# Performance work log

Measured on AMD Instinct MI355X. Metric: run time of the kernel, lower is better.

The kernel has to match this reference:

```python
import jax, jax.numpy as jnp
import numpy as np

B, D, H = 4096, 66, 512  # batch, system dim (22 atoms * 3), MLP hidden


def _dynamics(t, xs, W1, b1, W2, b2, W3, b3):
    # CNF vector field f(t, x): 3-layer SiLU MLP on concat([x, t])
    h = jnp.concatenate([xs, t], axis=1)          # [B, D+1]
    h = jax.nn.silu(h @ W1 + b1)                  # [B, H]
    h = jax.nn.silu(h @ W2 + b2)                  # [B, H]
    return h @ W3 + b3                            # [B, D]


def setup_inputs() -> dict:
    key = jax.random.key(0)
    ks = jax.random.split(key, 5)
    xs = jax.random.normal(ks[0], (B, D), dtype=jnp.float32)
    t = jax.random.uniform(ks[1], (B, 1), dtype=jnp.float32)
    W1 = jax.random.normal(ks[2], (D + 1, H), dtype=jnp.float32) / np.float32(np.sqrt(D + 1))
    b1 = jnp.zeros((H,), dtype=jnp.float32)
    W2 = jax.random.normal(ks[3], (H, H), dtype=jnp.float32) / np.float32(np.sqrt(H))
    b2 = jnp.zeros((H,), dtype=jnp.float32)
    W3 = jax.random.normal(ks[4], (H, D), dtype=jnp.float32) / np.float32(np.sqrt(H))
    b3 = jnp.zeros((D,), dtype=jnp.float32)
    return {"xs": xs, "t": t, "W1": W1, "b1": b1, "W2": W2, "b2": b2, "W3": W3, "b3": b3}


def reference(xs, t, W1, b1, W2, b2, W3, b3):
    # Exact divergence: trace of Jacobian d f / d x, computed with D JVPs
    # (forward-mode equivalent of the torch per-dim autograd.grad loop).
    def f(x):
        return _dynamics(t, x, W1, b1, W2, b2, W3, b3)

    dxs = f(xs)                                   # [B, D]
    eye = jnp.eye(D, dtype=xs.dtype)              # basis vectors e_i

    def jvp_col(e):
        _, tang = jax.jvp(f, (xs,), (jnp.broadcast_to(e, xs.shape),))
        return tang                               # J @ e_i, shape [B, D]

    tangs = jax.vmap(jvp_col)(eye)                # [D, B, D]
    div = jnp.einsum('dbd->b', tangs)             # sum_i (J e_i)_i = tr(J)
    return dxs, -div[:, None]
```

## Files before the change

kernel.cpp:

```cpp
#include <hip/hip_runtime.h>

#define Bn 4096
#define Dn 66
#define Hn 512

typedef __attribute__((ext_vector_type(8))) short short8;
typedef __attribute__((ext_vector_type(4))) float f32x4;

__device__ __forceinline__ unsigned short f2bf(float x) {
    union { float f; unsigned u; } v; v.f = x;
    unsigned r = v.u + 0x7fffu + ((v.u >> 16) & 1u);
    return (unsigned short)(r >> 16);
}
__device__ __forceinline__ float bf2f(unsigned short h) {
    union { float f; unsigned u; } v; v.u = ((unsigned)h) << 16; return v.f;
}


__global__ __launch_bounds__(512, 2) void k_pack(
    const float* __restrict__ W1, const float* __restrict__ W2,
    const float* __restrict__ W3,
    unsigned short* __restrict__ WQ, unsigned short* __restrict__ W3P)
{
    __shared__ float sLds[16*68];
    const int bid = blockIdx.x, tid = threadIdx.x;
    const int lane = tid & 63, wv = tid >> 6;

    if (bid < 64) {
        const int pb = bid;
        const int ct = pb >> 1;
        {
            const int r = tid >> 5, ii = tid & 31;
            const float* src = &W3[(size_t)(ct*16 + r)*Dn];
            sLds[r*68 + ii] = src[ii];
            sLds[r*68 + ii + 32] = src[ii + 32];
            if (ii < 2) sLds[r*68 + ii + 64] = src[ii + 64];
        }
        __syncthreads();
        const int ks = (pb & 1)*8 + wv;
        const int n = lane & 15, kg = lane >> 4;
        const int c = ct*16 + n;
        const int abase = ks*32 + kg*8;
        float w2v[8], m[8];
        #pragma unroll
        for (int j = 0; j < 8; ++j) {
            w2v[j] = W2[(size_t)(abase + j)*Hn + c];
            m[j] = 0.f;
        }
        #pragma unroll 2
        for (int i = 0; i < Dn; ++i) {
            const float w3 = sLds[n*68 + i];
            const float4 w1a = *(const float4*)&W1[(size_t)i*Hn + abase];
            const float4 w1b = *(const float4*)&W1[(size_t)i*Hn + abase + 4];
            m[0] = fmaf(w3, w1a.x, m[0]); m[1] = fmaf(w3, w1a.y, m[1]);
            m[2] = fmaf(w3, w1a.z, m[2]); m[3] = fmaf(w3, w1a.w, m[3]);
            m[4] = fmaf(w3, w1b.x, m[4]); m[5] = fmaf(w3, w1b.y, m[5]);
            m[6] = fmaf(w3, w1b.z, m[6]); m[7] = fmaf(w3, w1b.w, m[7]);
        }
        short8 pw, pc;
        #pragma unroll
        for (int j = 0; j < 8; ++j) {
            pw[j] = (short)f2bf(w2v[j]);
            pc[j] = (short)f2bf(w2v[j] * m[j]);
        }
        const size_t off = ((size_t)(ct*16 + ks)*64 + lane)*16;
        *(short8*)&WQ[off]     = pw;
        *(short8*)&WQ[off + 8] = pc;
    } else {
        const int tix = (bid - 64)*8 + wv;
        if (tix < 80) {
            const int ks = tix & 15;
            const int n = lane & 15;
            const int j_out = (tix >> 4)*16 + n;
            const int abase = ks*32 + (lane >> 4)*8;
            short8 p;
            #pragma unroll
            for (int j = 0; j < 8; ++j)
                p[j] = (j_out < Dn) ? (short)f2bf(W3[(size_t)(abase + j)*Dn + j_out]) : (short)0;
            *(short8*)&W3P[((size_t)tix*64 + lane)*8] = p;
        }
    }
}

__global__ __launch_bounds__(1024, 4) void k_fused(
    const float* __restrict__ xs, const float* __restrict__ tt,
    const float* __restrict__ W1, const float* __restrict__ b1,
    const unsigned short* __restrict__ WQ, const float* __restrict__ b2,
    const unsigned short* __restrict__ W3P, const float* __restrict__ b3,
    float* __restrict__ out)
{
    __shared__ float sX[67*16];
    __shared__ __align__(16) unsigned short sA[8192];
    __shared__ __align__(16) unsigned short sS[8192];
    __shared__ __align__(16) unsigned short sH[8192];
    __shared__ __align__(16) unsigned short sL[8192];
    __shared__ float sRed[16*16];

    const int tid = threadIdx.x, lane = tid & 63, wv = tid >> 6;
    const int rt = blockIdx.x, r0 = rt*16;
    const int n = lane & 15, kg = lane >> 4;
    const int rot = (rt >> 3) & 15;

    for (int idx = tid; idx < 67*16; idx += 1024) {
        const int i = idx >> 4, r = idx & 15;
        sX[idx] = (i < Dn) ? xs[(size_t)(r0+r)*Dn + i] : tt[r0+r];
    }
    __syncthreads();

    {
        const int rg = lane & 7, cg = lane >> 3;
        const int ks = wv;
        const int c0 = ks*32 + cg*4;
        const int irot = (rt >> 3) & 31;
        float z[2][4];
        {
            const float4 b4 = *(const float4*)&b1[c0];
            z[0][0]=b4.x; z[0][1]=b4.y; z[0][2]=b4.z; z[0][3]=b4.w;
            z[1][0]=b4.x; z[1][1]=b4.y; z[1][2]=b4.z; z[1][3]=b4.w;
        }
        #pragma unroll 2
        for (int s = 0; s < 67; ++s) {
            int i = s + irot; if (i >= 67) i -= 67;
            const float2 xf = *(const float2*)&sX[i*16 + 2*rg];
            const float4 wA = *(const float4*)&W1[(size_t)i*Hn + c0];
            const float ww[4] = {wA.x, wA.y, wA.z, wA.w};
            #pragma unroll
            for (int j = 0; j < 4; ++j) {
                z[0][j] = fmaf(xf.x, ww[j], z[0][j]);
                z[1][j] = fmaf(xf.y, ww[j], z[1][j]);
            }
        }
        const int kgrp = cg >> 1, joff = (cg & 1)*4;
        #pragma unroll
        for (int rr = 0; rr < 2; ++rr) {
            const int r = 2*rg + rr;
            ushort4 phi, ps;
            unsigned short* PH = (unsigned short*)&phi;
            unsigned short* PS = (unsigned short*)&ps;
            #pragma unroll
            for (int j = 0; j < 4; ++j) {
                const float zv = z[rr][j];
                const float sg = 1.f / (1.f + __expf(-zv));
                PH[j] = f2bf(zv * sg);
                PS[j] = f2bf(sg * (1.f + zv * (1.f - sg)));
            }
            const int off = ((ks)*64 + r + 16*kgrp)*8 + joff;
            *(ushort4*)&sA[off] = phi;
            *(ushort4*)&sS[off] = ps;
        }
    }
    __syncthreads();

    const int ctb = wv*2;
    f32x4 zac[2], vac[2];
    #pragma unroll
    for (int ti = 0; ti < 2; ++ti) {
        const float bz = b2[(ctb + ti)*16 + n];
        zac[ti] = (f32x4){bz, bz, bz, bz};
        vac[ti] = (f32x4){0.f, 0.f, 0.f, 0.f};
    }
    short8 wbuf[2][2], qbuf[2][2], abuf[2], sbuf[2];
    {
        const int ks0 = rot;
        abuf[0] = *(const short8*)&sA[(ks0*64 + lane)*8];
        sbuf[0] = *(const short8*)&sS[(ks0*64 + lane)*8];
        #pragma unroll
        for (int ti = 0; ti < 2; ++ti) {
            const size_t wo = ((size_t)((ctb + ti)*16 + ks0)*64 + lane)*16;
            wbuf[0][ti] = *(const short8*)&WQ[wo];
            qbuf[0][ti] = *(const short8*)&WQ[wo + 8];
        }
    }
    #pragma unroll
    for (int s = 0; s < 16; ++s) {
        const int cur = s & 1, nxt = cur ^ 1;
        if (s < 15) {
            const int ksn = (s + 1 + rot) & 15;
            abuf[nxt] = *(const short8*)&sA[(ksn*64 + lane)*8];
            sbuf[nxt] = *(const short8*)&sS[(ksn*64 + lane)*8];
            #pragma unroll
            for (int ti = 0; ti < 2; ++ti) {
                const size_t wo = ((size_t)((ctb + ti)*16 + ksn)*64 + lane)*16;
                wbuf[nxt][ti] = *(const short8*)&WQ[wo];
                qbuf[nxt][ti] = *(const short8*)&WQ[wo + 8];
            }
        }
        #pragma unroll
        for (int ti = 0; ti < 2; ++ti) {
            zac[ti] = __builtin_amdgcn_mfma_f32_16x16x32_bf16(abuf[cur], wbuf[cur][ti], zac[ti], 0, 0, 0);
            vac[ti] = __builtin_amdgcn_mfma_f32_16x16x32_bf16(sbuf[cur], qbuf[cur][ti], vac[ti], 0, 0, 0);
        }
    }

    float dp[4] = {0.f, 0.f, 0.f, 0.f};
    #pragma unroll
    for (int ti = 0; ti < 2; ++ti) {
        const int c = (ctb + ti)*16 + n;
        const int ks2 = c >> 5, kg2 = (c >> 3) & 3, j2 = c & 7;
        #pragma unroll
        for (int q = 0; q < 4; ++q) {
            const float z2 = zac[ti][q];
            const float sg = 1.f / (1.f + __expf(-z2));
            const float h2 = z2 * sg;
            dp[q] = fmaf(sg * (1.f + z2 * (1.f - sg)), vac[ti][q], dp[q]);
            const unsigned short hh = f2bf(h2);
            const int o = (ks2*64 + (kg*4 + q) + 16*kg2)*8 + j2;
            sH[o] = hh;
            sL[o] = f2bf(h2 - bf2f(hh));
        }
    }
    #pragma unroll
    for (int q = 0; q < 4; ++q) {
        float v = dp[q];
        v += __shfl_xor(v, 1, 64);
        v += __shfl_xor(v, 2, 64);
        v += __shfl_xor(v, 4, 64);
        v += __shfl_xor(v, 8, 64);
        if (n == 0) sRed[wv*16 + kg*4 + q] = v;
    }
    __syncthreads();

    if (tid < 16) {
        float s = 0.f;
        #pragma unroll
        for (int q = 0; q < 16; ++q) s += sRed[q*16 + tid];
        out[(size_t)Bn*Dn + r0 + tid] = -s;
    }

    if (wv < 5) {
        const int jt = wv;
        const int j = jt*16 + n;
        const float bj = (j < Dn) ? b3[j] : 0.f;
        f32x4 oac = (f32x4){bj, bj, bj, bj};
        #pragma unroll 4
        for (int s = 0; s < 16; ++s) {
            const int ks = (s + rot) & 15;
            const int aoff = (ks*64 + lane)*8;
            const short8 ahi = *(const short8*)&sH[aoff];
            const short8 alo = *(const short8*)&sL[aoff];
            const short8 wf  = *(const short8*)&W3P[((size_t)(jt*16 + ks)*64 + lane)*8];
            oac = __builtin_amdgcn_mfma_f32_16x16x32_bf16(ahi, wf, oac, 0, 0, 0);
            oac = __builtin_amdgcn_mfma_f32_16x16x32_bf16(alo, wf, oac, 0, 0, 0);
        }
        if (j < Dn) {
            #pragma unroll
            for (int q = 0; q < 4; ++q)
                out[(size_t)(r0 + kg*4 + q)*Dn + j] = oac[q];
        }
    }
}

extern "C" void kernel_launch(void* const* d_in, const int* in_sizes, int n_in,
                              void* d_out, int out_size, void* d_ws, size_t ws_size,
                              hipStream_t stream)
{
    const float* xs = (const float*)d_in[0];
    const float* t  = (const float*)d_in[1];
    const float* W1 = (const float*)d_in[2];
    const float* b1 = (const float*)d_in[3];
    const float* W2 = (const float*)d_in[4];
    const float* b2 = (const float*)d_in[5];
    const float* W3 = (const float*)d_in[6];
    const float* b3 = (const float*)d_in[7];
    float* out = (float*)d_out;

    char* ws = (char*)d_ws;
    unsigned short* WQ  = (unsigned short*)(ws);
    unsigned short* W3P = (unsigned short*)(ws + 1048576);

    k_pack <<<74,  512,  0, stream>>>(W1, W2, W3, WQ, W3P);
    k_fused<<<256, 1024, 0, stream>>>(xs, t, W1, b1, WQ, b2, W3P, b3, out);
}
```

Before: 106.7 us.

## Merge weight-packing kernel into fused kernel using cooperative grid sync

Folds the separate weight-packing pass (W2 scaled by W3·W1 products and the W3 bf16 packing) into the main fused kernel. The first few waves of each block do the packing, and a cooperative grid-wide barrier replaces the block barrier before the packed weights are read. This removes one kernel launch and its gap, and overlaps packing with the first-layer compute. The cost is a grid sync, a cooperative-launch requirement that all 256 blocks be co-resident, and uncoalesced W3 row reads that no longer go through shared memory.

```diff
diff --git a/kernel.cpp b/kernel.cpp
--- a/kernel.cpp
+++ b/kernel.cpp
@@ -1,4 +1,7 @@
 #include <hip/hip_runtime.h>
+#include <hip/hip_cooperative_groups.h>
+
+namespace cg = cooperative_groups;
 
 #define Bn 4096
 #define Dn 66
@@ -17,76 +20,12 @@
 }
 
 
-__global__ __launch_bounds__(512, 2) void k_pack(
-    const float* __restrict__ W1, const float* __restrict__ W2,
-    const float* __restrict__ W3,
-    unsigned short* __restrict__ WQ, unsigned short* __restrict__ W3P)
-{
-    __shared__ float sLds[16*68];
-    const int bid = blockIdx.x, tid = threadIdx.x;
-    const int lane = tid & 63, wv = tid >> 6;
-
-    if (bid < 64) {
-        const int pb = bid;
-        const int ct = pb >> 1;
-        {
-            const int r = tid >> 5, ii = tid & 31;
-            const float* src = &W3[(size_t)(ct*16 + r)*Dn];
-            sLds[r*68 + ii] = src[ii];
-            sLds[r*68 + ii + 32] = src[ii + 32];
-            if (ii < 2) sLds[r*68 + ii + 64] = src[ii + 64];
-        }
-        __syncthreads();
-        const int ks = (pb & 1)*8 + wv;
-        const int n = lane & 15, kg = lane >> 4;
-        const int c = ct*16 + n;
-        const int abase = ks*32 + kg*8;
-        float w2v[8], m[8];
-        #pragma unroll
-        for (int j = 0; j < 8; ++j) {
-            w2v[j] = W2[(size_t)(abase + j)*Hn + c];
-            m[j] = 0.f;
-        }
-        #pragma unroll 2
-        for (int i = 0; i < Dn; ++i) {
-            const float w3 = sLds[n*68 + i];
-            const float4 w1a = *(const float4*)&W1[(size_t)i*Hn + abase];
-            const float4 w1b = *(const float4*)&W1[(size_t)i*Hn + abase + 4];
-            m[0] = fmaf(w3, w1a.x, m[0]); m[1] = fmaf(w3, w1a.y, m[1]);
-            m[2] = fmaf(w3, w1a.z, m[2]); m[3] = fmaf(w3, w1a.w, m[3]);
-            m[4] = fmaf(w3, w1b.x, m[4]); m[5] = fmaf(w3, w1b.y, m[5]);
-            m[6] = fmaf(w3, w1b.z, m[6]); m[7] = fmaf(w3, w1b.w, m[7]);
-        }
-        short8 pw, pc;
-        #pragma unroll
-        for (int j = 0; j < 8; ++j) {
-            pw[j] = (short)f2bf(w2v[j]);
-            pc[j] = (short)f2bf(w2v[j] * m[j]);
-        }
-        const size_t off = ((size_t)(ct*16 + ks)*64 + lane)*16;
-        *(short8*)&WQ[off]     = pw;
-        *(short8*)&WQ[off + 8] = pc;
-    } else {
-        const int tix = (bid - 64)*8 + wv;
-        if (tix < 80) {
-            const int ks = tix & 15;
-            const int n = lane & 15;
-            const int j_out = (tix >> 4)*16 + n;
-            const int abase = ks*32 + (lane >> 4)*8;
-            short8 p;
-            #pragma unroll
-            for (int j = 0; j < 8; ++j)
-                p[j] = (j_out < Dn) ? (short)f2bf(W3[(size_t)(abase + j)*Dn + j_out]) : (short)0;
-            *(short8*)&W3P[((size_t)tix*64 + lane)*8] = p;
-        }
-    }
-}
-
-__global__ __launch_bounds__(1024, 4) void k_fused(
+__global__ __launch_bounds__(1024, 4) void k_all(
     const float* __restrict__ xs, const float* __restrict__ tt,
     const float* __restrict__ W1, const float* __restrict__ b1,
-    const unsigned short* __restrict__ WQ, const float* __restrict__ b2,
-    const unsigned short* __restrict__ W3P, const float* __restrict__ b3,
+    const float* __restrict__ W2, const float* __restrict__ b2,
+    const float* __restrict__ W3, const float* __restrict__ b3,
+    unsigned short* __restrict__ WQ, unsigned short* __restrict__ W3P,
     float* __restrict__ out)
 {
     __shared__ float sX[67*16];
@@ -106,6 +45,49 @@
         sX[idx] = (i < Dn) ? xs[(size_t)(r0+r)*Dn + i] : tt[r0+r];
     }
     __syncthreads();
+
+    if (wv < 2) {
+        const int tix = wv*256 + rt;
+        const int ct = tix >> 4, ks = tix & 15;
+        const int c = ct*16 + n;
+        const int abase = ks*32 + kg*8;
+        float w2v[8], m[8];
+        #pragma unroll
+        for (int j = 0; j < 8; ++j) {
+            w2v[j] = W2[(size_t)(abase + j)*Hn + c];
+            m[j] = 0.f;
+        }
+        const float* w3row = &W3[(size_t)c * Dn];
+        #pragma unroll 2
+        for (int i = 0; i < Dn; ++i) {
+            const float w3 = w3row[i];
+            const float4 w1a = *(const float4*)&W1[(size_t)i*Hn + abase];
+            const float4 w1b = *(const float4*)&W1[(size_t)i*Hn + abase + 4];
+            m[0] = fmaf(w3, w1a.x, m[0]); m[1] = fmaf(w3, w1a.y, m[1]);
+            m[2] = fmaf(w3, w1a.z, m[2]); m[3] = fmaf(w3, w1a.w, m[3]);
+            m[4] = fmaf(w3, w1b.x, m[4]); m[5] = fmaf(w3, w1b.y, m[5]);
+            m[6] = fmaf(w3, w1b.z, m[6]); m[7] = fmaf(w3, w1b.w, m[7]);
+        }
+        short8 pw, pc;
+        #pragma unroll
+        for (int j = 0; j < 8; ++j) {
+            pw[j] = (short)f2bf(w2v[j]);
+            pc[j] = (short)f2bf(w2v[j] * m[j]);
+        }
+        const size_t off = ((size_t)tix*64 + lane)*16;
+        *(short8*)&WQ[off]     = pw;
+        *(short8*)&WQ[off + 8] = pc;
+    } else if (wv == 2 && rt < 80) {
+        const int tix = rt;
+        const int ks = tix & 15;
+        const int j_out = (tix >> 4)*16 + n;
+        const int abase = ks*32 + kg*8;
+        short8 p;
+        #pragma unroll
+        for (int j = 0; j < 8; ++j)
+            p[j] = (j_out < Dn) ? (short)f2bf(W3[(size_t)(abase + j)*Dn + j_out]) : (short)0;
+        *(short8*)&W3P[((size_t)tix*64 + lane)*8] = p;
+    }
 
     {
         const int rg = lane & 7, cg = lane >> 3;
@@ -144,12 +126,13 @@
                 PH[j] = f2bf(zv * sg);
                 PS[j] = f2bf(sg * (1.f + zv * (1.f - sg)));
             }
-            const int off = ((ks)*64 + r + 16*kgrp)*8 + joff;
+            const int off = (ks*64 + r + 16*kgrp)*8 + joff;
             *(ushort4*)&sA[off] = phi;
             *(ushort4*)&sS[off] = ps;
         }
     }
-    __syncthreads();
+
+    cg::this_grid().sync();
 
     const int ctb = wv*2;
     f32x4 zac[2], vac[2];
@@ -268,6 +251,7 @@
     unsigned short* WQ  = (unsigned short*)(ws);
     unsigned short* W3P = (unsigned short*)(ws + 1048576);
 
-    k_pack <<<74,  512,  0, stream>>>(W1, W2, W3, WQ, W3P);
-    k_fused<<<256, 1024, 0, stream>>>(xs, t, W1, b1, WQ, b2, W3P, b3, out);
-}
+    void* args[] = {&xs, &t, &W1, &b1, &W2, &b2, &W3, &b3, &WQ, &W3P, &out};
+    hipLaunchCooperativeKernel((const void*)k_all, dim3(256), dim3(1024),
+                               args, 0, stream);
+}
```

After: 165.0 us. +54.7%, slower.

## Split weight-pack work finer and deepen MFMA operand prefetch pipelines

Applied to the files above, without the earlier changes.

The packing kernel is redistributed so each wave handles half a k-group (four columns instead of eight), reading W3 rows directly instead of staging them in LDS. This doubles the grid from 74 to 138 blocks to raise parallelism in the serial prep step. In the fused kernel the layer-2 operand prefetch goes from double to triple buffering, the layer-3 W3P loads get a double-buffered prefetch, and the layer-1 loop unroll is raised. Deeper buffering costs extra registers, which may lower occupancy.

```diff
diff --git a/kernel.cpp b/kernel.cpp
--- a/kernel.cpp
+++ b/kernel.cpp
@@ -22,63 +22,52 @@
     const float* __restrict__ W3,
     unsigned short* __restrict__ WQ, unsigned short* __restrict__ W3P)
 {
-    __shared__ float sLds[16*68];
-    const int bid = blockIdx.x, tid = threadIdx.x;
+    const int tid = threadIdx.x;
     const int lane = tid & 63, wv = tid >> 6;
-
-    if (bid < 64) {
-        const int pb = bid;
-        const int ct = pb >> 1;
-        {
-            const int r = tid >> 5, ii = tid & 31;
-            const float* src = &W3[(size_t)(ct*16 + r)*Dn];
-            sLds[r*68 + ii] = src[ii];
-            sLds[r*68 + ii + 32] = src[ii + 32];
-            if (ii < 2) sLds[r*68 + ii + 64] = src[ii + 64];
-        }
-        __syncthreads();
-        const int ks = (pb & 1)*8 + wv;
-        const int n = lane & 15, kg = lane >> 4;
+    const int task = blockIdx.x * 8 + wv;
+    const int n = lane & 15, kg = lane >> 4;
+
+    if (task < 1024) {
+        const int tix = task >> 1;
+        const int jh  = task & 1;
+        const int ct = tix >> 4, ks = tix & 15;
         const int c = ct*16 + n;
-        const int abase = ks*32 + kg*8;
-        float w2v[8], m[8];
-        #pragma unroll
-        for (int j = 0; j < 8; ++j) {
+        const int abase = ks*32 + kg*8 + jh*4;
+        float w2v[4], m[4];
+        #pragma unroll
+        for (int j = 0; j < 4; ++j) {
             w2v[j] = W2[(size_t)(abase + j)*Hn + c];
             m[j] = 0.f;
         }
-        #pragma unroll 2
+        const float* w3row = &W3[(size_t)c * Dn];
+        #pragma unroll 4
         for (int i = 0; i < Dn; ++i) {
-            const float w3 = sLds[n*68 + i];
+            const float w3 = w3row[i];
             const float4 w1a = *(const float4*)&W1[(size_t)i*Hn + abase];
-            const float4 w1b = *(const float4*)&W1[(size_t)i*Hn + abase + 4];
             m[0] = fmaf(w3, w1a.x, m[0]); m[1] = fmaf(w3, w1a.y, m[1]);
             m[2] = fmaf(w3, w1a.z, m[2]); m[3] = fmaf(w3, w1a.w, m[3]);
-            m[4] = fmaf(w3, w1b.x, m[4]); m[5] = fmaf(w3, w1b.y, m[5]);
-            m[6] = fmaf(w3, w1b.z, m[6]); m[7] = fmaf(w3, w1b.w, m[7]);
-        }
-        short8 pw, pc;
-        #pragma unroll
-        for (int j = 0; j < 8; ++j) {
-            pw[j] = (short)f2bf(w2v[j]);
-            pc[j] = (short)f2bf(w2v[j] * m[j]);
-        }
-        const size_t off = ((size_t)(ct*16 + ks)*64 + lane)*16;
-        *(short8*)&WQ[off]     = pw;
-        *(short8*)&WQ[off + 8] = pc;
-    } else {
-        const int tix = (bid - 64)*8 + wv;
-        if (tix < 80) {
-            const int ks = tix & 15;
-            const int n = lane & 15;
-            const int j_out = (tix >> 4)*16 + n;
-            const int abase = ks*32 + (lane >> 4)*8;
-            short8 p;
-            #pragma unroll
-            for (int j = 0; j < 8; ++j)
-                p[j] = (j_out < Dn) ? (short)f2bf(W3[(size_t)(abase + j)*Dn + j_out]) : (short)0;
-            *(short8*)&W3P[((size_t)tix*64 + lane)*8] = p;
-        }
+        }
+        ushort4 pw, pc;
+        unsigned short* PW = (unsigned short*)&pw;
+        unsigned short* PC = (unsigned short*)&pc;
+        #pragma unroll
+        for (int j = 0; j < 4; ++j) {
+            PW[j] = f2bf(w2v[j]);
+            PC[j] = f2bf(w2v[j] * m[j]);
+        }
+        const size_t off = ((size_t)tix*64 + lane)*16 + jh*4;
+        *(ushort4*)&WQ[off]     = pw;
+        *(ushort4*)&WQ[off + 8] = pc;
+    } else if (task < 1104) {
+        const int tix = task - 1024;
+        const int ks = tix & 15;
+        const int j_out = (tix >> 4)*16 + n;
+        const int abase = ks*32 + kg*8;
+        short8 p;
+        #pragma unroll
+        for (int j = 0; j < 8; ++j)
+            p[j] = (j_out < Dn) ? (short)f2bf(W3[(size_t)(abase + j)*Dn + j_out]) : (short)0;
+        *(short8*)&W3P[((size_t)tix*64 + lane)*8] = p;
     }
 }
 
@@ -118,7 +107,7 @@
             z[0][0]=b4.x; z[0][1]=b4.y; z[0][2]=b4.z; z[0][3]=b4.w;
             z[1][0]=b4.x; z[1][1]=b4.y; z[1][2]=b4.z; z[1][3]=b4.w;
         }
-        #pragma unroll 2
+        #pragma unroll 4
         for (int s = 0; s < 67; ++s) {
             int i = s + irot; if (i >= 67) i -= 67;
             const float2 xf = *(const float2*)&sX[i*16 + 2*rg];
@@ -144,7 +133,7 @@
                 PH[j] = f2bf(zv * sg);
                 PS[j] = f2bf(sg * (1.f + zv * (1.f - sg)));
             }
-            const int off = ((ks)*64 + r + 16*kgrp)*8 + joff;
+            const int off = (ks*64 + r + 16*kgrp)*8 + joff;
             *(ushort4*)&sA[off] = phi;
             *(ushort4*)&sS[off] = ps;
         }
@@ -159,36 +148,38 @@
         zac[ti] = (f32x4){bz, bz, bz, bz};
         vac[ti] = (f32x4){0.f, 0.f, 0.f, 0.f};
     }
-    short8 wbuf[2][2], qbuf[2][2], abuf[2], sbuf[2];
-    {
-        const int ks0 = rot;
-        abuf[0] = *(const short8*)&sA[(ks0*64 + lane)*8];
-        sbuf[0] = *(const short8*)&sS[(ks0*64 + lane)*8];
+    short8 wA[3][2], wQ[3][2], aR[3], sR[3];
+    #pragma unroll
+    for (int p = 0; p < 2; ++p) {
+        const int ksp = (p + rot) & 15;
+        aR[p] = *(const short8*)&sA[(ksp*64 + lane)*8];
+        sR[p] = *(const short8*)&sS[(ksp*64 + lane)*8];
         #pragma unroll
         for (int ti = 0; ti < 2; ++ti) {
-            const size_t wo = ((size_t)((ctb + ti)*16 + ks0)*64 + lane)*16;
-            wbuf[0][ti] = *(const short8*)&WQ[wo];
-            qbuf[0][ti] = *(const short8*)&WQ[wo + 8];
+            const size_t wo = ((size_t)((ctb + ti)*16 + ksp)*64 + lane)*16;
+            wA[p][ti] = *(const short8*)&WQ[wo];
+            wQ[p][ti] = *(const short8*)&WQ[wo + 8];
         }
     }
     #pragma unroll
     for (int s = 0; s < 16; ++s) {
-        const int cur = s & 1, nxt = cur ^ 1;
-        if (s < 15) {
-            const int ksn = (s + 1 + rot) & 15;
-            abuf[nxt] = *(const short8*)&sA[(ksn*64 + lane)*8];
-            sbuf[nxt] = *(const short8*)&sS[(ksn*64 + lane)*8];
+        const int cur = s % 3;
+        if (s < 14) {
+            const int nx = (s + 2) % 3;
+            const int ksn = (s + 2 + rot) & 15;
+            aR[nx] = *(const short8*)&sA[(ksn*64 + lane)*8];
+            sR[nx] = *(const short8*)&sS[(ksn*64 + lane)*8];
             #pragma unroll
             for (int ti = 0; ti < 2; ++ti) {
                 const size_t wo = ((size_t)((ctb + ti)*16 + ksn)*64 + lane)*16;
-                wbuf[nxt][ti] = *(const short8*)&WQ[wo];
-                qbuf[nxt][ti] = *(const short8*)&WQ[wo + 8];
+                wA[nx][ti] = *(const short8*)&WQ[wo];
+                wQ[nx][ti] = *(const short8*)&WQ[wo + 8];
             }
         }
         #pragma unroll
         for (int ti = 0; ti < 2; ++ti) {
-            zac[ti] = __builtin_amdgcn_mfma_f32_16x16x32_bf16(abuf[cur], wbuf[cur][ti], zac[ti], 0, 0, 0);
-            vac[ti] = __builtin_amdgcn_mfma_f32_16x16x32_bf16(sbuf[cur], qbuf[cur][ti], vac[ti], 0, 0, 0);
+            zac[ti] = __builtin_amdgcn_mfma_f32_16x16x32_bf16(aR[cur], wA[cur][ti], zac[ti], 0, 0, 0);
+            vac[ti] = __builtin_amdgcn_mfma_f32_16x16x32_bf16(sR[cur], wQ[cur][ti], vac[ti], 0, 0, 0);
         }
     }
 
@@ -232,15 +223,21 @@
         const int j = jt*16 + n;
         const float bj = (j < Dn) ? b3[j] : 0.f;
         f32x4 oac = (f32x4){bj, bj, bj, bj};
-        #pragma unroll 4
+        short8 wf[2];
+        wf[0] = *(const short8*)&W3P[((size_t)(jt*16 + rot)*64 + lane)*8];
+        #pragma unroll
         for (int s = 0; s < 16; ++s) {
+            const int cur = s & 1;
+            if (s < 15) {
+                const int ksn = (s + 1 + rot) & 15;
+                wf[cur ^ 1] = *(const short8*)&W3P[((size_t)(jt*16 + ksn)*64 + lane)*8];
+            }
             const int ks = (s + rot) & 15;
             const int aoff = (ks*64 + lane)*8;
             const short8 ahi = *(const short8*)&sH[aoff];
             const short8 alo = *(const short8*)&sL[aoff];
-            const short8 wf  = *(const short8*)&W3P[((size_t)(jt*16 + ks)*64 + lane)*8];
-            oac = __builtin_amdgcn_mfma_f32_16x16x32_bf16(ahi, wf, oac, 0, 0, 0);
-            oac = __builtin_amdgcn_mfma_f32_16x16x32_bf16(alo, wf, oac, 0, 0, 0);
+            oac = __builtin_amdgcn_mfma_f32_16x16x32_bf16(ahi, wf[cur], oac, 0, 0, 0);
+            oac = __builtin_amdgcn_mfma_f32_16x16x32_bf16(alo, wf[cur], oac, 0, 0, 0);
         }
         if (j < Dn) {
             #pragma unroll
@@ -268,6 +265,6 @@
     unsigned short* WQ  = (unsigned short*)(ws);
     unsigned short* W3P = (unsigned short*)(ws + 1048576);
 
-    k_pack <<<74,  512,  0, stream>>>(W1, W2, W3, WQ, W3P);
+    k_pack <<<138, 512,  0, stream>>>(W1, W2, W3, WQ, W3P);
     k_fused<<<256, 1024, 0, stream>>>(xs, t, W1, b1, WQ, b2, W3P, b3, out);
 }
```

After: 104.1 us. -2.4%, faster.
